# Kernel tuning notes

Hardware: AMD Instinct MI355X
Metric: run time of the kernel (lower is better)

Reference implementation:

```python
import jax, jax.numpy as jnp
import numpy as np

NUM_CLASSES = 10
CLAUSES_PER_CLASS = 100  # first half vote positive, second half negative
M = NUM_CLASSES * CLAUSES_PER_CLASS  # 1000 clauses
D = 1152   # 2*C*kh*kw literals (pos+neg) per patch
L = 676    # patches (26x26)
B = 64
MASK_DENSITY = 0.01  # ~11 selected literals per clause


def setup_inputs() -> dict:
    key = jax.random.key(0)
    k1, k2, k3 = jax.random.split(key, 3)
    # binary literals in {0,1}
    literals = jax.random.randint(k1, (B, D, L), 0, 2, dtype=jnp.int32)
    # fixed discrete clause definitions: sparse boolean selection over D literals
    clause_mask = jax.random.uniform(k2, (M, D)) < MASK_DENSITY
    # per-clause vote weight alpha (learnable parameter in the torch module)
    alpha = 1.0 + 0.1 * jax.random.normal(k3, (M,), dtype=jnp.float32)
    return {"literals": literals, "clause_mask": clause_mask, "alpha": alpha}


def reference(literals, clause_mask, alpha):
    # literals: [B, D, L] in {0,1}; clause_mask: [M, D] bool; alpha: [M]
    lits = literals.astype(jnp.float32)
    mask = clause_mask.astype(jnp.float32)
    # AND over selected literals: clause m fires at patch l iff every selected
    # literal is 1  <=>  sum of selected literal values == number selected.
    sel_count = jnp.einsum('md,bdl->bml', mask, lits)      # [B, M, L]
    n_sel = mask.sum(axis=1)                               # [M]
    fired = sel_count >= n_sel[None, :, None]              # [B, M, L] bool (empty clause fires)
    # OR across patches
    or_patches = jnp.any(fired, axis=2).astype(alpha.dtype)  # [B, M]
    # weighted vote: per class, first half of its clauses vote +, second half -
    weighted = (or_patches * alpha[None, :]).reshape(-1, NUM_CLASSES, CLAUSES_PER_CLASS)
    half = CLAUSES_PER_CLASS // 2
    sign = jnp.concatenate([jnp.ones((half,), jnp.float32),
                            -jnp.ones((half,), jnp.float32)])
    scores = (weighted * sign).sum(axis=-1)                # [B, num_classes]
    return scores
```

## Files before the change

kernel.cpp:

```cpp
#include <hip/hip_runtime.h>
#include <hip/hip_bf16.h>
#include <stdint.h>

#define NUM_CLASSES 10
#define CPC 100
#define M_CLAUSES 1000
#define D_LITS 1152
#define L_PATCHES 676
#define BATCH 64
#define KMAX 64
#define NW 12

typedef unsigned long long u64;

__global__ void zero_flag_kernel(int* flag) { *flag = 0; }

__global__ void detect_kernel(const unsigned int* __restrict__ mask_u32, int n_u32,
                              int* __restrict__ flag) {
  int i = blockIdx.x * blockDim.x + threadIdx.x;
  int stride = gridDim.x * blockDim.x;
  int local = 0;
  for (; i < n_u32; i += stride) {
    if (mask_u32[i] & 0xFFFFFF00u) local = 1;
  }
  if (local) atomicOr(flag, 1);
}

__global__ void mask_index_kernel(const void* __restrict__ maskp,
                                  const int* __restrict__ flag,
                                  int* __restrict__ counts,
                                  int* __restrict__ idx) {
  int m = blockIdx.x;
  __shared__ int cnt;
  if (threadIdx.x == 0) cnt = 0;
  __syncthreads();
  bool isbool = (*flag != 0);
  for (int d = threadIdx.x; d < D_LITS; d += blockDim.x) {
    bool sel;
    if (isbool) sel = ((const unsigned char*)maskp)[(size_t)m * D_LITS + d] != 0;
    else        sel = ((const int*)maskp)[(size_t)m * D_LITS + d] != 0;
    if (sel) {
      int p = atomicAdd(&cnt, 1);
      if (p < KMAX) idx[m * KMAX + p] = d;
    }
  }
  __syncthreads();
  if (threadIdx.x == 0) counts[m] = cnt > KMAX ? KMAX : cnt;
}

__global__ __launch_bounds__(256) void pack_kernel(const int* __restrict__ lits,
                                                   u64* __restrict__ packed) {
  int wib  = threadIdx.x >> 6;
  int lane = threadIdx.x & 63;
  int row  = blockIdx.x * 4 + wib;
  if (row >= BATCH * D_LITS) return;
  const int4* src = (const int4*)(lits + (size_t)row * L_PATCHES);
  u64 w[12];
#pragma unroll
  for (int it = 0; it < 3; ++it) {
    int i4 = it * 64 + lane;
    int4 v = make_int4(0, 0, 0, 0);
    if (i4 < (L_PATCHES / 4)) v = src[i4];
    w[it * 4 + 0] = __ballot(v.x != 0);
    w[it * 4 + 1] = __ballot(v.y != 0);
    w[it * 4 + 2] = __ballot(v.z != 0);
    w[it * 4 + 3] = __ballot(v.w != 0);
  }
  if (lane == 0) {
    ulonglong2* d2 = (ulonglong2*)(packed + (size_t)row * NW);
    d2[0] = make_ulonglong2(w[0],  w[1]);
    d2[1] = make_ulonglong2(w[2],  w[3]);
    d2[2] = make_ulonglong2(w[4],  w[5]);
    d2[3] = make_ulonglong2(w[6],  w[7]);
    d2[4] = make_ulonglong2(w[8],  w[9]);
    d2[5] = make_ulonglong2(w[10], w[11]);
  }
}

__global__ __launch_bounds__(256) void score_kernel(const u64* __restrict__ packed,
                                                    const int* __restrict__ counts,
                                                    const int* __restrict__ idx,
                                                    const float* __restrict__ alpha,
                                                    float* __restrict__ out) {
  int b = blockIdx.x;
  __shared__ float cls[NUM_CLASSES];
  if (threadIdx.x < NUM_CLASSES) cls[threadIdx.x] = 0.f;
  __syncthreads();
  const u64* base = packed + (size_t)b * D_LITS * NW;
  const u64 TAIL = (1ull << 41) - 1;
  for (int m = threadIdx.x; m < M_CLAUSES; m += blockDim.x) {
    int c = counts[m];
    u64 a0 = ~0ull, a1 = ~0ull, a2 = ~0ull, a3 = ~0ull;
    u64 a4 = ~0ull, a5 = ~0ull, a6 = ~0ull, a7 = ~0ull;
    u64 a8 = TAIL,  a9 = TAIL,  a10 = TAIL, a11 = TAIL;
    const int* il = idx + m * KMAX;
    for (int k = 0; k < c; ++k) {
      const ulonglong2* row = (const ulonglong2*)(base + (size_t)il[k] * NW);
      ulonglong2 r0 = row[0], r1 = row[1], r2 = row[2];
      ulonglong2 r3 = row[3], r4 = row[4], r5 = row[5];
      a0 &= r0.x;  a1 &= r0.y;  a2 &= r1.x;  a3 &= r1.y;
      a4 &= r2.x;  a5 &= r2.y;  a6 &= r3.x;  a7 &= r3.y;
      a8 &= r4.x;  a9 &= r4.y;  a10 &= r5.x; a11 &= r5.y;
    }
    u64 any = (a0 | a1 | a2 | a3) | (a4 | a5 | a6 | a7) | (a8 | a9 | a10 | a11);
    if (any) {
      float a = alpha[m];
      int cid = m / CPC;
      int q = m - cid * CPC;
      atomicAdd(&cls[cid], (q < (CPC / 2)) ? a : -a);
    }
  }
  __syncthreads();
  if (threadIdx.x < NUM_CLASSES) out[b * NUM_CLASSES + threadIdx.x] = cls[threadIdx.x];
}

extern "C" void kernel_launch(void* const* d_in, const int* in_sizes, int n_in,
                              void* d_out, int out_size, void* d_ws, size_t ws_size,
                              hipStream_t stream) {
  const int*   lits  = (const int*)d_in[0];
  const void*  mask  = d_in[1];
  const float* alpha = (const float*)d_in[2];
  float* out = (float*)d_out;

  char* ws = (char*)d_ws;
  int*  flag   = (int*)ws;
  int*  counts = (int*)(ws + 256);
  int*  idx    = (int*)(ws + 4352);
  u64*  packed = (u64*)(ws + 262144);

  zero_flag_kernel<<<1, 1, 0, stream>>>(flag);
  detect_kernel<<<512, 256, 0, stream>>>((const unsigned int*)mask,
                                         (M_CLAUSES * D_LITS) / 4, flag);
  mask_index_kernel<<<M_CLAUSES, 256, 0, stream>>>(mask, flag, counts, idx);
  pack_kernel<<<(BATCH * D_LITS) / 4, 256, 0, stream>>>(lits, packed);
  score_kernel<<<BATCH, 256, 0, stream>>>(packed, counts, idx, alpha, out);
}
```

Before: 319.7 us.

## Fuse setup kernels into pack, transpose packed layout, parallelize scoring over clauses

Merges flag zeroing, mask-type detection and output zeroing into the pack kernel launch, cutting five launches down to two. The packed bitmask is re-laid out as [d][word-pair][batch] so that, in a new score kernel with one block per clause and one thread per batch, loads are coalesced across the 64 batch lanes. Mask index building moves into the score kernel, and class scores are accumulated with global atomics. This exposes 1000 blocks of parallelism instead of 64 and removes the scattered per-thread row gathers, at the cost of global atomic contention on the output.

```diff
diff --git a/kernel.cpp b/kernel.cpp
--- a/kernel.cpp
+++ b/kernel.cpp
@@ -9,109 +9,114 @@
 #define L_PATCHES 676
 #define BATCH 64
 #define KMAX 64
-#define NW 12
+#define NPACK_BLK 18432
+#define NDET_BLK 64
 
 typedef unsigned long long u64;
 
-__global__ void zero_flag_kernel(int* flag) { *flag = 0; }
-
-__global__ void detect_kernel(const unsigned int* __restrict__ mask_u32, int n_u32,
-                              int* __restrict__ flag) {
-  int i = blockIdx.x * blockDim.x + threadIdx.x;
-  int stride = gridDim.x * blockDim.x;
-  int local = 0;
-  for (; i < n_u32; i += stride) {
-    if (mask_u32[i] & 0xFFFFFF00u) local = 1;
-  }
-  if (local) atomicOr(flag, 1);
-}
-
-__global__ void mask_index_kernel(const void* __restrict__ maskp,
-                                  const int* __restrict__ flag,
-                                  int* __restrict__ counts,
-                                  int* __restrict__ idx) {
-  int m = blockIdx.x;
-  __shared__ int cnt;
-  if (threadIdx.x == 0) cnt = 0;
-  __syncthreads();
-  bool isbool = (*flag != 0);
-  for (int d = threadIdx.x; d < D_LITS; d += blockDim.x) {
-    bool sel;
-    if (isbool) sel = ((const unsigned char*)maskp)[(size_t)m * D_LITS + d] != 0;
-    else        sel = ((const int*)maskp)[(size_t)m * D_LITS + d] != 0;
-    if (sel) {
-      int p = atomicAdd(&cnt, 1);
-      if (p < KMAX) idx[m * KMAX + p] = d;
+__global__ __launch_bounds__(256) void pack_kernel(
+    const int* __restrict__ lits,
+    const unsigned int* __restrict__ mask_u32,
+    ulonglong2* __restrict__ packed,
+    int* __restrict__ flags,
+    float* __restrict__ out)
+{
+  int bid = blockIdx.x;
+  if (bid < NPACK_BLK) {
+    int wib  = threadIdx.x >> 6;
+    int lane = threadIdx.x & 63;
+    int row  = bid * 4 + wib;
+    int b = row / D_LITS;
+    int d = row - b * D_LITS;
+    const int4* src = (const int4*)(lits + (size_t)row * L_PATCHES);
+    u64 w0,w1,w2,w3,w4,w5,w6,w7,w8,w9,w10,w11;
+    {
+      int4 v = src[lane];
+      w0 = __ballot(v.x != 0); w1 = __ballot(v.y != 0);
+      w2 = __ballot(v.z != 0); w3 = __ballot(v.w != 0);
     }
-  }
-  __syncthreads();
-  if (threadIdx.x == 0) counts[m] = cnt > KMAX ? KMAX : cnt;
-}
-
-__global__ __launch_bounds__(256) void pack_kernel(const int* __restrict__ lits,
-                                                   u64* __restrict__ packed) {
-  int wib  = threadIdx.x >> 6;
-  int lane = threadIdx.x & 63;
-  int row  = blockIdx.x * 4 + wib;
-  if (row >= BATCH * D_LITS) return;
-  const int4* src = (const int4*)(lits + (size_t)row * L_PATCHES);
-  u64 w[12];
-#pragma unroll
-  for (int it = 0; it < 3; ++it) {
-    int i4 = it * 64 + lane;
-    int4 v = make_int4(0, 0, 0, 0);
-    if (i4 < (L_PATCHES / 4)) v = src[i4];
-    w[it * 4 + 0] = __ballot(v.x != 0);
-    w[it * 4 + 1] = __ballot(v.y != 0);
-    w[it * 4 + 2] = __ballot(v.z != 0);
-    w[it * 4 + 3] = __ballot(v.w != 0);
-  }
-  if (lane == 0) {
-    ulonglong2* d2 = (ulonglong2*)(packed + (size_t)row * NW);
-    d2[0] = make_ulonglong2(w[0],  w[1]);
-    d2[1] = make_ulonglong2(w[2],  w[3]);
-    d2[2] = make_ulonglong2(w[4],  w[5]);
-    d2[3] = make_ulonglong2(w[6],  w[7]);
-    d2[4] = make_ulonglong2(w[8],  w[9]);
-    d2[5] = make_ulonglong2(w[10], w[11]);
+    {
+      int4 v = src[64 + lane];
+      w4 = __ballot(v.x != 0); w5 = __ballot(v.y != 0);
+      w6 = __ballot(v.z != 0); w7 = __ballot(v.w != 0);
+    }
+    {
+      int4 v = make_int4(0,0,0,0);
+      if (lane < 41) v = src[128 + lane];
+      w8 = __ballot(v.x != 0); w9 = __ballot(v.y != 0);
+      w10 = __ballot(v.z != 0); w11 = __ballot(v.w != 0);
+    }
+    ulonglong2* dst = packed + (size_t)d * 6 * 64 + b;
+    if      (lane == 0) dst[0*64] = make_ulonglong2(w0,  w1);
+    else if (lane == 1) dst[1*64] = make_ulonglong2(w2,  w3);
+    else if (lane == 2) dst[2*64] = make_ulonglong2(w4,  w5);
+    else if (lane == 3) dst[3*64] = make_ulonglong2(w6,  w7);
+    else if (lane == 4) dst[4*64] = make_ulonglong2(w8,  w9);
+    else if (lane == 5) dst[5*64] = make_ulonglong2(w10, w11);
+  } else if (bid < NPACK_BLK + NDET_BLK) {
+    int db = bid - NPACK_BLK;
+    __shared__ int sfound;
+    if (threadIdx.x == 0) sfound = 0;
+    __syncthreads();
+    int n = (M_CLAUSES * D_LITS) / 4;
+    int found = 0;
+    for (int i = db * 256 + threadIdx.x; i < n; i += NDET_BLK * 256)
+      if (mask_u32[i] & 0xFFFFFF00u) found = 1;
+    if (found) sfound = 1;
+    __syncthreads();
+    if (threadIdx.x == 0) flags[db] = sfound;
+  } else {
+    for (int i = threadIdx.x; i < BATCH * NUM_CLASSES; i += 256) out[i] = 0.f;
   }
 }
 
-__global__ __launch_bounds__(256) void score_kernel(const u64* __restrict__ packed,
-                                                    const int* __restrict__ counts,
-                                                    const int* __restrict__ idx,
-                                                    const float* __restrict__ alpha,
-                                                    float* __restrict__ out) {
-  int b = blockIdx.x;
-  __shared__ float cls[NUM_CLASSES];
-  if (threadIdx.x < NUM_CLASSES) cls[threadIdx.x] = 0.f;
-  __syncthreads();
-  const u64* base = packed + (size_t)b * D_LITS * NW;
-  const u64 TAIL = (1ull << 41) - 1;
-  for (int m = threadIdx.x; m < M_CLAUSES; m += blockDim.x) {
-    int c = counts[m];
-    u64 a0 = ~0ull, a1 = ~0ull, a2 = ~0ull, a3 = ~0ull;
-    u64 a4 = ~0ull, a5 = ~0ull, a6 = ~0ull, a7 = ~0ull;
-    u64 a8 = TAIL,  a9 = TAIL,  a10 = TAIL, a11 = TAIL;
-    const int* il = idx + m * KMAX;
-    for (int k = 0; k < c; ++k) {
-      const ulonglong2* row = (const ulonglong2*)(base + (size_t)il[k] * NW);
-      ulonglong2 r0 = row[0], r1 = row[1], r2 = row[2];
-      ulonglong2 r3 = row[3], r4 = row[4], r5 = row[5];
-      a0 &= r0.x;  a1 &= r0.y;  a2 &= r1.x;  a3 &= r1.y;
-      a4 &= r2.x;  a5 &= r2.y;  a6 &= r3.x;  a7 &= r3.y;
-      a8 &= r4.x;  a9 &= r4.y;  a10 &= r5.x; a11 &= r5.y;
-    }
-    u64 any = (a0 | a1 | a2 | a3) | (a4 | a5 | a6 | a7) | (a8 | a9 | a10 | a11);
-    if (any) {
-      float a = alpha[m];
-      int cid = m / CPC;
-      int q = m - cid * CPC;
-      atomicAdd(&cls[cid], (q < (CPC / 2)) ? a : -a);
-    }
+__global__ __launch_bounds__(64) void score_kernel(
+    const ulonglong2* __restrict__ packed,
+    const void* __restrict__ maskp,
+    const int* __restrict__ flags,
+    const float* __restrict__ alpha,
+    float* __restrict__ out)
+{
+  int m   = blockIdx.x;
+  int tid = threadIdx.x;
+  __shared__ int list[KMAX];
+  __shared__ int cnt;
+  __shared__ int isbool;
+  if (tid == 0) {
+    cnt = 0;
+    int f = 0;
+#pragma unroll
+    for (int i = 0; i < NDET_BLK; ++i) f |= flags[i];
+    isbool = f;
   }
   __syncthreads();
-  if (threadIdx.x < NUM_CLASSES) out[b * NUM_CLASSES + threadIdx.x] = cls[threadIdx.x];
+  bool ib = (isbool != 0);
+  for (int d = tid; d < D_LITS; d += 64) {
+    bool sel = ib ? (((const unsigned char*)maskp)[(size_t)m * D_LITS + d] != 0)
+                  : (((const int*)maskp)[(size_t)m * D_LITS + d] != 0);
+    if (sel) { int p = atomicAdd(&cnt, 1); if (p < KMAX) list[p] = d; }
+  }
+  __syncthreads();
+  int c = cnt; if (c > KMAX) c = KMAX;
+  const u64 TAIL = (1ull << 41) - 1;
+  u64 a0=~0ull,a1=~0ull,a2=~0ull,a3=~0ull,a4=~0ull,a5=~0ull,a6=~0ull,a7=~0ull;
+  u64 a8=TAIL, a9=TAIL, a10=TAIL, a11=TAIL;
+  for (int k = 0; k < c; ++k) {
+    int d = list[k];
+    const ulonglong2* p = packed + (size_t)d * 6 * 64 + tid;
+    ulonglong2 r0 = p[0*64], r1 = p[1*64], r2 = p[2*64];
+    ulonglong2 r3 = p[3*64], r4 = p[4*64], r5 = p[5*64];
+    a0 &= r0.x;  a1 &= r0.y;  a2 &= r1.x;  a3 &= r1.y;
+    a4 &= r2.x;  a5 &= r2.y;  a6 &= r3.x;  a7 &= r3.y;
+    a8 &= r4.x;  a9 &= r4.y;  a10 &= r5.x; a11 &= r5.y;
+  }
+  u64 any = (a0|a1|a2|a3)|(a4|a5|a6|a7)|(a8|a9|a10|a11);
+  if (any) {
+    float a = alpha[m];
+    int cid = m / CPC;
+    float v = ((m - cid * CPC) < (CPC / 2)) ? a : -a;
+    atomicAdd(&out[tid * NUM_CLASSES + cid], v);
+  }
 }
 
 extern "C" void kernel_launch(void* const* d_in, const int* in_sizes, int n_in,
@@ -123,15 +128,10 @@
   float* out = (float*)d_out;
 
   char* ws = (char*)d_ws;
-  int*  flag   = (int*)ws;
-  int*  counts = (int*)(ws + 256);
-  int*  idx    = (int*)(ws + 4352);
-  u64*  packed = (u64*)(ws + 262144);
+  int*        flags  = (int*)ws;
+  ulonglong2* packed = (ulonglong2*)(ws + 4096);
 
-  zero_flag_kernel<<<1, 1, 0, stream>>>(flag);
-  detect_kernel<<<512, 256, 0, stream>>>((const unsigned int*)mask,
-                                         (M_CLAUSES * D_LITS) / 4, flag);
-  mask_index_kernel<<<M_CLAUSES, 256, 0, stream>>>(mask, flag, counts, idx);
-  pack_kernel<<<(BATCH * D_LITS) / 4, 256, 0, stream>>>(lits, packed);
-  score_kernel<<<BATCH, 256, 0, stream>>>(packed, counts, idx, alpha, out);
+  pack_kernel<<<NPACK_BLK + NDET_BLK + 1, 256, 0, stream>>>(
+      lits, (const unsigned int*)mask, packed, flags, out);
+  score_kernel<<<M_CLAUSES, 64, 0, stream>>>(packed, mask, flags, alpha, out);
 }
```

Result: faster. 296.9 us (-7.1%).
